# Kernel tuning notes

Hardware: AMD Instinct MI355X
Metric: run time of the kernel (lower is better)

The kernel has to match this reference:

```python
import jax, jax.numpy as jnp
import numpy as np

N, E, F_IN, F_OUT = 50000, 640000, 128, 128


def setup_inputs() -> dict:
    key = jax.random.key(0)
    k_x, k_w, k_b = jax.random.split(key, 3)
    x = jax.random.normal(k_x, (N, F_IN), dtype=jnp.float32)
    # Unique directed edges so segment_sum == dense spmm with adj[u,v]=1.
    rng = np.random.default_rng(0)
    lin = np.unique(rng.integers(0, N * N, size=2 * E, dtype=np.int64))[:E]
    edge_index = jnp.stack([jnp.asarray(lin // N), jnp.asarray(lin % N)]).astype(jnp.int64)
    stdv = 1.0 / np.sqrt(F_OUT).astype(np.float32)
    weight = jax.random.uniform(k_w, (F_IN, F_OUT), dtype=jnp.float32, minval=-stdv, maxval=stdv)
    bias = jax.random.uniform(k_b, (F_OUT,), dtype=jnp.float32, minval=-stdv, maxval=stdv)
    return {"input": x, "edge_index": edge_index, "weight": weight, "bias": bias}


def reference(input, edge_index, weight, bias):
    # support = X @ W  [N, F_OUT]
    support = input @ weight
    # Dense adj with adj[u,v]=1 followed by spmm(adj, support) is, for unique
    # edges, exactly: out[u] = sum_{(u,v) in edges} support[v]
    u, v = edge_index[0], edge_index[1]
    out = jax.ops.segment_sum(support[v], u, num_segments=input.shape[0])
    return out + bias
```

## Files before the change

### kernel.cpp

```cpp
#include <hip/hip_runtime.h>
#include <stdint.h>


typedef __attribute__((ext_vector_type(8))) short bf16x8;
typedef __attribute__((ext_vector_type(4))) float f32x4;

#define WSTRIDE 136

__device__ __forceinline__ unsigned short f2bf(float f) {
    union { float f; uint32_t u; } c; c.f = f;
    uint32_t u = c.u;
    uint32_t r = (u + 0x7FFFu + ((u >> 16) & 1u)) >> 16;
    return (unsigned short)r;
}

__global__ __launch_bounds__(256)
void gcn_setup(const int* __restrict__ eu, const float* __restrict__ W,
               int* __restrict__ row_ptr, unsigned short* __restrict__ Wg,
               int N, int E)
{
    const int g = blockIdx.x * 256 + threadIdx.x;
    if (g < E) {
        int cur  = eu[g];
        int prev = (g > 0) ? eu[g - 1] : -1;
        for (int r = prev + 1; r <= cur; ++r) row_ptr[r] = g;
    }
    if (g <= N) {
        int last = eu[E - 1];
        if (g > last) row_ptr[g] = E;
    }
    if (g < 16384) {
        int k = g >> 7, n = g & 127;
        Wg[n * 128 + k] = f2bf(W[g]);
    }
}

__global__ __launch_bounds__(256)
void gcn_main(const float* __restrict__ x,
              const int* __restrict__ ev,
              const int* __restrict__ row_ptr,
              const unsigned short* __restrict__ Wg,
              const float* __restrict__ bias,
              float* __restrict__ out,
              int N, int E, int TW)
{
    __shared__ __align__(16) unsigned short At[2][16 * WSTRIDE];

    const int t    = threadIdx.x;
    const int wid  = t >> 6;
    const int lane = t & 63;
    const int quad = lane >> 4;
    const int l15  = lane & 15;
    const int half = lane >> 5;
    const int l31  = lane & 31;

    const int wg = blockIdx.x * 4 + wid;

    int bnd;
    {
        const int m8 = lane & 7;
        const int e8 = (lane >> 3) & 1;
        const int ridx = min(wg + m8 * TW + e8, N);
        bnd = row_ptr[ridx];
    }

    unsigned short* Am = &At[wid >> 1][(wid & 1) * 8 * WSTRIDE];
    const float4* x4 = (const float4*)x;

    int vIdx = ev[min(__shfl(bnd, 0) + lane, E - 1)];

    for (int m = 0; m < 8; ++m) {
        const int s = __shfl(bnd, m);
        const int c = __shfl(bnd, m + 8) - s;
        int vNext = (m < 7) ? ev[min(__shfl(bnd, m + 1) + lane, E - 1)] : 0;

        float4 acc0 = {0.f, 0.f, 0.f, 0.f};
        float4 acc1 = {0.f, 0.f, 0.f, 0.f};
        for (int base = 0; base < c; base += 16) {
            if (base && ((base & 63) == 0))
                vIdx = ev[min(s + base + lane, E - 1)];
            const int boff = base & 63;
            float4 tv[8];
            float  sc[8];
            #pragma unroll
            for (int k = 0; k < 8; ++k) {
                const int eidx = base + 2 * k + half;
                const int slot = (boff + 2 * k + half) & 63;
                int v = __shfl(vIdx, slot);
                const bool act = (eidx < c);
                sc[k] = act ? 1.0f : 0.0f;
                v = act ? v : 0;
                tv[k] = x4[((long long)v << 5) + l31];
            }
            #pragma unroll
            for (int k = 0; k < 8; ++k) {
                float4& a = (k & 1) ? acc1 : acc0;
                a.x = fmaf(tv[k].x, sc[k], a.x);
                a.y = fmaf(tv[k].y, sc[k], a.y);
                a.z = fmaf(tv[k].z, sc[k], a.z);
                a.w = fmaf(tv[k].w, sc[k], a.w);
            }
        }
        vIdx = vNext;

        acc0.x += acc1.x; acc0.y += acc1.y; acc0.z += acc1.z; acc0.w += acc1.w;
        acc0.x += __shfl_xor(acc0.x, 32);
        acc0.y += __shfl_xor(acc0.y, 32);
        acc0.z += __shfl_xor(acc0.z, 32);
        acc0.w += __shfl_xor(acc0.w, 32);
        if (half == 0) {
            ushort4 pk;
            pk.x = f2bf(acc0.x); pk.y = f2bf(acc0.y);
            pk.z = f2bf(acc0.z); pk.w = f2bf(acc0.w);
            *(ushort4*)(Am + m * WSTRIDE + 4 * l31) = pk;
        }
    }
    __syncthreads();

    const int p  = wid >> 1;
    const int ch = wid & 1;
    const unsigned short* Ar = &At[p][0];
    f32x4 acc[4];
    #pragma unroll
    for (int nt = 0; nt < 4; ++nt) { acc[nt].x = 0.f; acc[nt].y = 0.f; acc[nt].z = 0.f; acc[nt].w = 0.f; }

    #pragma unroll
    for (int ks = 0; ks < 4; ++ks) {
        const int kofs = ks * 32 + quad * 8;
        bf16x8 a = *(const bf16x8*)(Ar + l15 * WSTRIDE + kofs);
        #pragma unroll
        for (int nt = 0; nt < 4; ++nt) {
            const int col = ch * 64 + nt * 16 + l15;
            bf16x8 b = *(const bf16x8*)(Wg + col * 128 + kofs);
            acc[nt] = __builtin_amdgcn_mfma_f32_16x16x32_bf16(a, b, acc[nt], 0, 0, 0);
        }
    }

    const int wgpair = blockIdx.x * 4 + 2 * p;
    #pragma unroll
    for (int nt = 0; nt < 4; ++nt) {
        const int col = ch * 64 + nt * 16 + l15;
        const float bcol = bias[col];
        #pragma unroll
        for (int r = 0; r < 4; ++r) {
            const int mi  = quad * 4 + r;
            const int row = wgpair + (mi >> 3) + (mi & 7) * TW;
            if (row < N)
                __builtin_nontemporal_store(acc[nt][r] + bcol,
                                            &out[(long long)row * 128 + col]);
        }
    }
}

extern "C" void kernel_launch(void* const* d_in, const int* in_sizes, int n_in,
                              void* d_out, int out_size, void* d_ws, size_t ws_size,
                              hipStream_t stream) {
    const float* x    = (const float*)d_in[0];
    const int*   ei   = (const int*)d_in[1];
    const float* W    = (const float*)d_in[2];
    const float* bias = (const float*)d_in[3];
    float*       out  = (float*)d_out;

    const int N = in_sizes[0] / 128;
    const int E = in_sizes[1] / 2;

    int*            row_ptr = (int*)d_ws;
    unsigned short* Wg      = (unsigned short*)((char*)d_ws + (((size_t)(N + 1) * 4 + 255) & ~(size_t)255));

    const int setup_threads = (E > N + 1 ? E : N + 1);
    gcn_setup<<<(setup_threads + 255) / 256, 256, 0, stream>>>(ei, W, row_ptr, Wg, N, E);

    const int grid = (N + 31) / 32;
    const int TW   = grid * 4;
    gcn_main<<<grid, 256, 0, stream>>>(x, ei + E, row_ptr, Wg, bias, out, N, E, TW);
}
```

Before: 134.2 us.

## Gather neighbor features from a bf16 copy of x and halve rows per block

Adds a cast kernel that writes x to bf16 in the workspace. The aggregation then gathers 16-byte bf16 rows instead of fp32, halving gather traffic, and each wave covers 4 rows instead of 8 with a grid twice as large. Each wave's MFMA now computes 32 output columns of one 16-row tile. This adds an extra pass over x (read fp32, write bf16) and rounds the inputs before accumulation, which loosens precision. It falls back to the fp32 path if the workspace is too small.

```diff
diff --git a/kernel.cpp b/kernel.cpp
--- a/kernel.cpp
+++ b/kernel.cpp
@@ -12,6 +12,10 @@
     uint32_t u = c.u;
     uint32_t r = (u + 0x7FFFu + ((u >> 16) & 1u)) >> 16;
     return (unsigned short)r;
+}
+__device__ __forceinline__ float bf2f(unsigned short u) {
+    union { uint32_t u; float f; } c; c.u = ((uint32_t)u) << 16;
+    return c.f;
 }
 
 __global__ __launch_bounds__(256)
@@ -36,7 +40,23 @@
 }
 
 __global__ __launch_bounds__(256)
+void gcn_cast(const float* __restrict__ x, unsigned short* __restrict__ xb, int n8)
+{
+    const int g = blockIdx.x * 256 + threadIdx.x;
+    if (g < n8) {
+        const float4* x4 = (const float4*)x;
+        float4 a = x4[2 * g], b = x4[2 * g + 1];
+        union { unsigned short u[8]; uint4 v; } pk;
+        pk.u[0] = f2bf(a.x); pk.u[1] = f2bf(a.y); pk.u[2] = f2bf(a.z); pk.u[3] = f2bf(a.w);
+        pk.u[4] = f2bf(b.x); pk.u[5] = f2bf(b.y); pk.u[6] = f2bf(b.z); pk.u[7] = f2bf(b.w);
+        ((uint4*)xb)[g] = pk.v;
+    }
+}
+
+template<bool BF>
+__global__ __launch_bounds__(256)
 void gcn_main(const float* __restrict__ x,
+              const unsigned short* __restrict__ xb,
               const int* __restrict__ ev,
               const int* __restrict__ row_ptr,
               const unsigned short* __restrict__ Wg,
@@ -44,107 +64,139 @@
               float* __restrict__ out,
               int N, int E, int TW)
 {
-    __shared__ __align__(16) unsigned short At[2][16 * WSTRIDE];
+    __shared__ __align__(16) unsigned short At[16 * WSTRIDE];
 
     const int t    = threadIdx.x;
     const int wid  = t >> 6;
     const int lane = t & 63;
     const int quad = lane >> 4;
     const int l15  = lane & 15;
-    const int half = lane >> 5;
-    const int l31  = lane & 31;
 
     const int wg = blockIdx.x * 4 + wid;
 
     int bnd;
     {
-        const int m8 = lane & 7;
-        const int e8 = (lane >> 3) & 1;
-        const int ridx = min(wg + m8 * TW + e8, N);
-        bnd = row_ptr[ridx];
-    }
-
-    unsigned short* Am = &At[wid >> 1][(wid & 1) * 8 * WSTRIDE];
-    const float4* x4 = (const float4*)x;
+        const int m = (lane >> 1) & 3, e = lane & 1;
+        bnd = row_ptr[min(wg + m * TW + e, N)];
+    }
+
+    unsigned short* Am = At + (wid * 4) * WSTRIDE;
 
     int vIdx = ev[min(__shfl(bnd, 0) + lane, E - 1)];
 
-    for (int m = 0; m < 8; ++m) {
-        const int s = __shfl(bnd, m);
-        const int c = __shfl(bnd, m + 8) - s;
-        int vNext = (m < 7) ? ev[min(__shfl(bnd, m + 1) + lane, E - 1)] : 0;
-
-        float4 acc0 = {0.f, 0.f, 0.f, 0.f};
-        float4 acc1 = {0.f, 0.f, 0.f, 0.f};
-        for (int base = 0; base < c; base += 16) {
-            if (base && ((base & 63) == 0))
-                vIdx = ev[min(s + base + lane, E - 1)];
-            const int boff = base & 63;
-            float4 tv[8];
-            float  sc[8];
+    for (int m = 0; m < 4; ++m) {
+        const int s = __shfl(bnd, 2 * m);
+        const int c = __shfl(bnd, 2 * m + 1) - s;
+        int vNext = (m < 3) ? ev[min(__shfl(bnd, 2 * m + 2) + lane, E - 1)] : 0;
+
+        if constexpr (BF) {
+            const int eslot = lane >> 4;
+            const int fo = l15 * 8;
+            float fa[8];
             #pragma unroll
-            for (int k = 0; k < 8; ++k) {
-                const int eidx = base + 2 * k + half;
-                const int slot = (boff + 2 * k + half) & 63;
-                int v = __shfl(vIdx, slot);
-                const bool act = (eidx < c);
-                sc[k] = act ? 1.0f : 0.0f;
-                v = act ? v : 0;
-                tv[k] = x4[((long long)v << 5) + l31];
+            for (int i = 0; i < 8; ++i) fa[i] = 0.f;
+
+            for (int base = 0; base < c; base += 32) {
+                if (base && ((base & 63) == 0))
+                    vIdx = ev[min(s + base + lane, E - 1)];
+                bf16x8 tv[8];
+                float  sc[8];
+                #pragma unroll
+                for (int k = 0; k < 8; ++k) {
+                    const int eidx = base + k * 4 + eslot;
+                    int v = __shfl(vIdx, eidx & 63);
+                    const bool act = (eidx < c);
+                    sc[k] = act ? 1.0f : 0.0f;
+                    v = act ? v : 0;
+                    tv[k] = *(const bf16x8*)(xb + (size_t)v * 128 + fo);
+                }
+                #pragma unroll
+                for (int k = 0; k < 8; ++k)
+                    #pragma unroll
+                    for (int i = 0; i < 8; ++i)
+                        fa[i] = fmaf(bf2f((unsigned short)tv[k][i]), sc[k], fa[i]);
             }
             #pragma unroll
-            for (int k = 0; k < 8; ++k) {
-                float4& a = (k & 1) ? acc1 : acc0;
-                a.x = fmaf(tv[k].x, sc[k], a.x);
-                a.y = fmaf(tv[k].y, sc[k], a.y);
-                a.z = fmaf(tv[k].z, sc[k], a.z);
-                a.w = fmaf(tv[k].w, sc[k], a.w);
+            for (int i = 0; i < 8; ++i) {
+                fa[i] += __shfl_xor(fa[i], 16);
+                fa[i] += __shfl_xor(fa[i], 32);
+            }
+            if (eslot == 0) {
+                union { unsigned short u[8]; uint4 v; } pk;
+                #pragma unroll
+                for (int i = 0; i < 8; ++i) pk.u[i] = f2bf(fa[i]);
+                *(uint4*)(Am + m * WSTRIDE + fo) = pk.v;
+            }
+        } else {
+            const int half = lane >> 5;
+            const int l31  = lane & 31;
+            const float4* x4 = (const float4*)x;
+            const float4 fz = {0.f, 0.f, 0.f, 0.f};
+            float4 a0 = fz, a1 = fz;
+            for (int base = 0; base < c; base += 16) {
+                if (base && ((base & 63) == 0))
+                    vIdx = ev[min(s + base + lane, E - 1)];
+                float4 tv[8];
+                float  sc[8];
+                #pragma unroll
+                for (int k = 0; k < 8; ++k) {
+                    const int eidx = base + 2 * k + half;
+                    int v = __shfl(vIdx, eidx & 63);
+                    const bool act = (eidx < c);
+                    sc[k] = act ? 1.0f : 0.0f;
+                    v = act ? v : 0;
+                    tv[k] = x4[((long long)v << 5) + l31];
+                }
+                #pragma unroll
+                for (int k = 0; k < 8; ++k) {
+                    float4& a = (k & 1) ? a1 : a0;
+                    a.x = fmaf(tv[k].x, sc[k], a.x);
+                    a.y = fmaf(tv[k].y, sc[k], a.y);
+                    a.z = fmaf(tv[k].z, sc[k], a.z);
+                    a.w = fmaf(tv[k].w, sc[k], a.w);
+                }
+            }
+            a0.x += a1.x; a0.y += a1.y; a0.z += a1.z; a0.w += a1.w;
+            a0.x += __shfl_xor(a0.x, 32);
+            a0.y += __shfl_xor(a0.y, 32);
+            a0.z += __shfl_xor(a0.z, 32);
+            a0.w += __shfl_xor(a0.w, 32);
+            if (half == 0) {
+                ushort4 pk;
+                pk.x = f2bf(a0.x); pk.y = f2bf(a0.y);
+                pk.z = f2bf(a0.z); pk.w = f2bf(a0.w);
+                *(ushort4*)(Am + m * WSTRIDE + 4 * l31) = pk;
             }
         }
         vIdx = vNext;
-
-        acc0.x += acc1.x; acc0.y += acc1.y; acc0.z += acc1.z; acc0.w += acc1.w;
-        acc0.x += __shfl_xor(acc0.x, 32);
-        acc0.y += __shfl_xor(acc0.y, 32);
-        acc0.z += __shfl_xor(acc0.z, 32);
-        acc0.w += __shfl_xor(acc0.w, 32);
-        if (half == 0) {
-            ushort4 pk;
-            pk.x = f2bf(acc0.x); pk.y = f2bf(acc0.y);
-            pk.z = f2bf(acc0.z); pk.w = f2bf(acc0.w);
-            *(ushort4*)(Am + m * WSTRIDE + 4 * l31) = pk;
-        }
     }
     __syncthreads();
 
-    const int p  = wid >> 1;
-    const int ch = wid & 1;
-    const unsigned short* Ar = &At[p][0];
-    f32x4 acc[4];
+    f32x4 acc[2];
     #pragma unroll
-    for (int nt = 0; nt < 4; ++nt) { acc[nt].x = 0.f; acc[nt].y = 0.f; acc[nt].z = 0.f; acc[nt].w = 0.f; }
+    for (int nt = 0; nt < 2; ++nt) { acc[nt].x = 0.f; acc[nt].y = 0.f; acc[nt].z = 0.f; acc[nt].w = 0.f; }
 
     #pragma unroll
     for (int ks = 0; ks < 4; ++ks) {
         const int kofs = ks * 32 + quad * 8;
-        bf16x8 a = *(const bf16x8*)(Ar + l15 * WSTRIDE + kofs);
+        bf16x8 a = *(const bf16x8*)(At + l15 * WSTRIDE + kofs);
         #pragma unroll
-        for (int nt = 0; nt < 4; ++nt) {
-            const int col = ch * 64 + nt * 16 + l15;
+        for (int nt = 0; nt < 2; ++nt) {
+            const int col = wid * 32 + nt * 16 + l15;
             bf16x8 b = *(const bf16x8*)(Wg + col * 128 + kofs);
             acc[nt] = __builtin_amdgcn_mfma_f32_16x16x32_bf16(a, b, acc[nt], 0, 0, 0);
         }
     }
 
-    const int wgpair = blockIdx.x * 4 + 2 * p;
+    const int b4 = blockIdx.x * 4;
     #pragma unroll
-    for (int nt = 0; nt < 4; ++nt) {
-        const int col = ch * 64 + nt * 16 + l15;
+    for (int nt = 0; nt < 2; ++nt) {
+        const int col = wid * 32 + nt * 16 + l15;
         const float bcol = bias[col];
         #pragma unroll
         for (int r = 0; r < 4; ++r) {
             const int mi  = quad * 4 + r;
-            const int row = wgpair + (mi >> 3) + (mi & 7) * TW;
+            const int row = b4 + (mi >> 2) + (mi & 3) * TW;
             if (row < N)
                 __builtin_nontemporal_store(acc[nt][r] + bcol,
                                             &out[(long long)row * 128 + col]);
@@ -164,13 +216,26 @@
     const int N = in_sizes[0] / 128;
     const int E = in_sizes[1] / 2;
 
+    const size_t rp_b   = ((size_t)(N + 1) * 4 + 255) & ~(size_t)255;
+    const size_t wg_off = rp_b;
+    const size_t xb_off = (wg_off + 32768 + 255) & ~(size_t)255;
+    const size_t xb_b   = (size_t)N * 128 * 2;
+
     int*            row_ptr = (int*)d_ws;
-    unsigned short* Wg      = (unsigned short*)((char*)d_ws + (((size_t)(N + 1) * 4 + 255) & ~(size_t)255));
+    unsigned short* Wg      = (unsigned short*)((char*)d_ws + wg_off);
+    unsigned short* xb      = (unsigned short*)((char*)d_ws + xb_off);
+    const bool use_bf = (ws_size >= xb_off + xb_b);
 
     const int setup_threads = (E > N + 1 ? E : N + 1);
     gcn_setup<<<(setup_threads + 255) / 256, 256, 0, stream>>>(ei, W, row_ptr, Wg, N, E);
 
-    const int grid = (N + 31) / 32;
+    const int grid = (N + 15) / 16;
     const int TW   = grid * 4;
-    gcn_main<<<grid, 256, 0, stream>>>(x, ei + E, row_ptr, Wg, bias, out, N, E, TW);
-}
+    if (use_bf) {
+        const int n8 = N * 16;
+        gcn_cast<<<(n8 + 255) / 256, 256, 0, stream>>>(x, xb, n8);
+        gcn_main<true><<<grid, 256, 0, stream>>>(x, xb, ei + E, row_ptr, Wg, bias, out, N, E, TW);
+    } else {
+        gcn_main<false><<<grid, 256, 0, stream>>>(x, xb, ei + E, row_ptr, Wg, bias, out, N, E, TW);
+    }
+}
```

Result: faster. 124.8 us (-7.0%).
